# Optimization experiments

Measured on AMD Instinct MI355X. Metric: run time of the kernel, lower is better.

## Reference

```python
import jax, jax.numpy as jnp
import numpy as np

D_MODEL = 1024
N_HEADS = 16
K_TOP = 64
D_HEAD = D_MODEL // N_HEADS


def setup_inputs() -> dict:
    key = jax.random.key(0)
    ks = jax.random.split(key, 9)
    B, L = 8, 4096
    bound = 1.0 / np.sqrt(D_MODEL)  # nn.Linear default init range
    lin = lambda k: jax.random.uniform(k, (D_MODEL, D_MODEL), jnp.float32, -bound, bound)
    vec = lambda k: jax.random.uniform(k, (D_MODEL,), jnp.float32, -bound, bound)
    return {
        "query": jax.random.normal(ks[0], (B, L, D_MODEL), jnp.float32),
        "Wq": lin(ks[1]), "bq": vec(ks[2]),
        "Wk": lin(ks[3]), "bk": vec(ks[4]),
        "Wv": lin(ks[5]), "bv": vec(ks[6]),
        "Wo": lin(ks[7]), "bo": vec(ks[8]),
    }


def reference(query, Wq, bq, Wk, bk, Wv, bv, Wo, bo):
    B, L_q, D = query.shape
    L_k = L_q  # self-attention: key = value = query
    F_q = L_q // 2 + 1
    F_k = L_k // 2 + 1
    k_top = min(K_TOP, F_q)

    def proj(x, W, b):
        # (B, L, D) -> (B, H, L, d_head)
        return (x @ W + b).reshape(B, -1, N_HEADS, D_HEAD).transpose(0, 2, 1, 3)

    q = proj(query, Wq, bq)
    k = proj(query, Wk, bk)
    v = proj(query, Wv, bv)

    q_freq = jnp.fft.rfft(q, axis=2)  # (B, H, F_q, d_head) complex64
    k_freq = jnp.fft.rfft(k, axis=2)
    v_freq = jnp.fft.rfft(v, axis=2)

    # top-k frequency bins by mean spectral magnitude of the query
    q_energy = jnp.abs(q_freq).mean(axis=-1)  # (B, H, F_q)
    _, idx = jax.lax.top_k(q_energy, k_top)   # (B, H, k)
    mapped_idx = jnp.clip(
        jnp.round(idx.astype(jnp.float32) * (F_k - 1) / (F_q - 1)).astype(jnp.int32),
        0, F_k - 1)

    gather = lambda x, i: jnp.take_along_axis(x, i[..., None], axis=2)
    q_top = gather(q_freq, idx)          # (B, H, k, d_head)
    k_top_freq = gather(k_freq, mapped_idx)
    v_top = gather(v_freq, mapped_idx)

    eps = 1e-8
    attn_score = (q_top.real * k_top_freq.real).sum(-1) / (D_HEAD ** 0.5 + eps)
    attn = jax.nn.softmax(attn_score, axis=-1)[..., None]  # (B, H, k, 1)

    # fill spectrum with mean of query spectrum, then scatter attended bins
    q_mean_freq = q_freq.mean(axis=2, keepdims=True)  # (B, H, 1, d_head) complex
    out_freq = jnp.broadcast_to(q_mean_freq, (B, N_HEADS, F_q, D_HEAD))
    src = (attn * v_top.real).astype(out_freq.dtype)  # real -> complex (imag=0)
    bi = jnp.arange(B)[:, None, None]
    hi = jnp.arange(N_HEADS)[None, :, None]
    out_freq = out_freq.at[bi, hi, idx].set(src)

    out_time = jnp.fft.irfft(out_freq, n=L_q, axis=2)  # (B, H, L, d_head)
    out = out_time.transpose(0, 2, 1, 3).reshape(B, L_q, D)
    return out @ Wo + bo
```

## Files before the change

### kernel.cpp

```cpp
#include <hip/hip_runtime.h>
#include <math.h>
#include <stdint.h>


typedef _Float16 f16;
typedef _Float16 f16x8 __attribute__((ext_vector_type(8)));
typedef float f32x4 __attribute__((ext_vector_type(4)));

#define PI_F 3.14159265358979323846f
#define PADJ(j) ((j) + ((j) >> 3))

__device__ __forceinline__ void gl_lds16(const void* g, void* l) {
  __builtin_amdgcn_global_load_lds((const __attribute__((address_space(1))) void*)g,
                                   (__attribute__((address_space(3))) void*)l, 16, 0, 0);
}

__device__ __forceinline__ float2 cadd(float2 a, float2 b) { return make_float2(a.x + b.x, a.y + b.y); }
__device__ __forceinline__ float2 csub(float2 a, float2 b) { return make_float2(a.x - b.x, a.y - b.y); }
__device__ __forceinline__ float2 cmul(float2 a, float2 b) {
  return make_float2(a.x * b.x - a.y * b.y, a.x * b.y + a.y * b.x);
}
__device__ __forceinline__ float2 cmni(float2 a) { return make_float2(a.y, -a.x); }

__device__ __forceinline__ void stg4(const char* g, size_t stride, int kb, char* lds,
                                     int tid, int w, int swz) {
#pragma unroll
  for (int it = 0; it < 4; ++it) {
    int row = it * 32 + (tid >> 3);
    gl_lds16(g + (size_t)row * stride + kb + swz, lds + it * 4096 + w * 1024);
  }
}

__global__ __launch_bounds__(256) void k_tw(float2* __restrict__ twtab, float2* __restrict__ utab) {
  int j = blockIdx.x * 256 + threadIdx.x;
  if (j < 2048) {
    float ang = (float)j * (-6.28318530717958647692f / 2048.0f);
    twtab[j] = make_float2(cosf(ang), sinf(ang));
  } else if (j < 4097) {
    int f = j - 2048;
    float ang = (float)f * (-6.28318530717958647692f / 4096.0f);
    utab[f] = make_float2(cosf(ang), sinf(ang));
  }
}

__global__ __launch_bounds__(256) void k_prep(const float* __restrict__ Wq, const float* __restrict__ Wo,
                                              f16* __restrict__ WqT, f16* __restrict__ WoT) {
  __shared__ float t[32][33];
  const float* src = blockIdx.z ? Wo : Wq;
  f16* dst = blockIdx.z ? WoT : WqT;
  int c0 = blockIdx.x * 32, r0 = blockIdx.y * 32;
  int tx = threadIdx.x, ty = threadIdx.y;
#pragma unroll
  for (int yy = 0; yy < 4; ++yy)
    t[ty + yy * 8][tx] = src[(size_t)(r0 + ty + yy * 8) * 1024 + c0 + tx];
  __syncthreads();
#pragma unroll
  for (int yy = 0; yy < 4; ++yy)
    dst[(size_t)(c0 + ty + yy * 8) * 1024 + r0 + tx] = (f16)t[tx][ty + yy * 8];
}

__global__ __launch_bounds__(256) void k_prep2(const float* __restrict__ Wk, const float* __restrict__ Wv,
                                               f16* __restrict__ WkT, f16* __restrict__ WvT) {
  __shared__ float t[32][33];
  const float* src = blockIdx.z ? Wv : Wk;
  f16* dst = blockIdx.z ? WvT : WkT;
  int c0 = blockIdx.x * 32, r0 = blockIdx.y * 32;
  int tx = threadIdx.x, ty = threadIdx.y;
#pragma unroll
  for (int yy = 0; yy < 4; ++yy)
    t[ty + yy * 8][tx] = src[(size_t)(r0 + ty + yy * 8) * 1024 + c0 + tx];
  __syncthreads();
#pragma unroll
  for (int yy = 0; yy < 4; ++yy)
    dst[(size_t)(c0 + ty + yy * 8) * 1024 + r0 + tx] = (f16)t[tx][ty + yy * 8];
}

__global__ __launch_bounds__(256) void k_t1(const float* __restrict__ X, float* __restrict__ Xt) {
  __shared__ float t[32][33];
  int b = blockIdx.z;
  int l0 = blockIdx.x * 32, d0 = blockIdx.y * 32;
  int tx = threadIdx.x, ty = threadIdx.y;
#pragma unroll
  for (int yy = 0; yy < 4; ++yy)
    t[ty + yy * 8][tx] = X[((size_t)b * 4096 + l0 + ty + yy * 8) * 1024 + d0 + tx];
  __syncthreads();
#pragma unroll
  for (int yy = 0; yy < 4; ++yy)
    Xt[((size_t)b * 1024 + d0 + ty + yy * 8) * 4096 + l0 + tx] = t[tx][ty + yy * 8];
}

__device__ __forceinline__ void r8_stage(const float2* __restrict__ cur, float2* __restrict__ nxt,
                                         const float2* __restrict__ tw, int tid, int lg) {
  int Ls = 1 << lg;
  int p = tid >> lg, q = tid & (Ls - 1);
  float2 x[8];
#pragma unroll
  for (int u = 0; u < 8; ++u) x[u] = cur[PADJ(tid + 256 * u)];
  float2 s0 = cadd(x[0], x[4]), d0v = csub(x[0], x[4]);
  float2 s1 = cadd(x[2], x[6]), d1v = csub(x[2], x[6]);
  float2 e0 = cadd(s0, s1), e2 = csub(s0, s1);
  float2 md1 = cmni(d1v);
  float2 e1 = cadd(d0v, md1), e3 = csub(d0v, md1);
  float2 t0 = cadd(x[1], x[5]), u0 = csub(x[1], x[5]);
  float2 t1 = cadd(x[3], x[7]), u1 = csub(x[3], x[7]);
  float2 o0 = cadd(t0, t1), o2 = csub(t0, t1);
  float2 mu1 = cmni(u1);
  float2 o1 = cadd(u0, mu1), o3 = csub(u0, mu1);
  const float C8 = 0.70710678118654752440f;
  float2 w1 = make_float2(C8 * (o1.x + o1.y), C8 * (o1.y - o1.x));
  float2 w2 = cmni(o2);
  float2 w3 = make_float2(C8 * (o3.y - o3.x), -C8 * (o3.x + o3.y));
  float2 y[8];
  y[0] = cadd(e0, o0); y[4] = csub(e0, o0);
  y[1] = cadd(e1, w1); y[5] = csub(e1, w1);
  y[2] = cadd(e2, w2); y[6] = csub(e2, w2);
  y[3] = cadd(e3, w3); y[7] = csub(e3, w3);
  int tb = p << lg;
#pragma unroll
  for (int v = 1; v < 8; ++v) y[v] = cmul(y[v], tw[tb * v]);
  int ob = q + (p << (lg + 3));
#pragma unroll
  for (int v = 0; v < 8; ++v) nxt[PADJ(ob + (v << lg))] = y[v];
}

__global__ __launch_bounds__(256) void k_fft(const float* __restrict__ Xt,
                                             const float2* __restrict__ twtab,
                                             const float2* __restrict__ utab,
                                             f16* __restrict__ PReU, f16* __restrict__ PImU,
                                             float* __restrict__ sumXf) {
  __shared__ float2 bufA[2304];
  __shared__ float2 bufB[2304];
  __shared__ float redr[256], redi[256];
  int tid = threadIdx.x;
  int blk = blockIdx.x;

  const float4* src = (const float4*)(Xt + (size_t)blk * 4096);
#pragma unroll
  for (int r = 0; r < 4; ++r) {
    int i4 = r * 256 + tid;
    float4 v = src[i4];
    bufA[PADJ(2 * i4)] = make_float2(v.x, v.y);
    bufA[PADJ(2 * i4 + 1)] = make_float2(v.z, v.w);
  }
  __syncthreads();
  r8_stage(bufA, bufB, twtab, tid, 0);
  __syncthreads();
  r8_stage(bufB, bufA, twtab, tid, 3);
  __syncthreads();
  r8_stage(bufA, bufB, twtab, tid, 6);
  __syncthreads();
#pragma unroll
  for (int h = 0; h < 2; ++h) {
    int i = (h << 8) + tid;
    float2 a0 = bufB[PADJ(i)], a1 = bufB[PADJ(i + 512)];
    float2 a2 = bufB[PADJ(i + 1024)], a3 = bufB[PADJ(i + 1536)];
    float2 s02 = cadd(a0, a2), d02 = csub(a0, a2);
    float2 s13 = cadd(a1, a3), d13m = cmni(csub(a1, a3));
    bufA[PADJ(i)] = cadd(s02, s13);
    bufA[PADJ(i + 512)] = cadd(d02, d13m);
    bufA[PADJ(i + 1024)] = csub(s02, s13);
    bufA[PADJ(i + 1536)] = csub(d02, d13m);
  }
  __syncthreads();
  float sumr = 0.f, sumi = 0.f;
  size_t obase = (size_t)blk * 2049;
  for (int f = tid; f <= 2048; f += 256) {
    int fz = f & 2047, fm = (2048 - f) & 2047;
    float2 z = bufA[PADJ(fz)], m = bufA[PADJ(fm)];
    float Er = 0.5f * (z.x + m.x), Ei = 0.5f * (z.y - m.y);
    float Or = 0.5f * (z.y + m.y), Oi = -0.5f * (z.x - m.x);
    float2 wv = utab[f];
    float Xr = Er + wv.x * Or - wv.y * Oi;
    float Xi = Ei + wv.x * Oi + wv.y * Or;
    PReU[obase + f] = (f16)Xr;
    PImU[obase + f] = (f16)Xi;
    sumr += Xr; sumi += Xi;
  }
  __syncthreads();
  redr[tid] = sumr; redi[tid] = sumi;
  __syncthreads();
  for (int s = 128; s > 0; s >>= 1) {
    if (tid < s) { redr[tid] += redr[tid + s]; redi[tid] += redi[tid + s]; }
    __syncthreads();
  }
  if (tid == 0) { sumXf[2 * blk] = redr[0]; sumXf[2 * blk + 1] = redi[0]; }
}

__global__ __launch_bounds__(256) void k_C(const float* __restrict__ sumXf, const float* __restrict__ Wq,
                                           const float* __restrict__ bq,
                                           float* __restrict__ Cre, float* __restrict__ Cim) {
  int b = blockIdx.x >> 2;
  int hd = ((blockIdx.x & 3) << 8) + threadIdx.x;
  float accr = 0.f, acci = 0.f;
  for (int dm = 0; dm < 1024; ++dm) {
    float w = Wq[(size_t)dm * 1024 + hd];
    accr += sumXf[2 * (b * 1024 + dm)] * w;
    acci += sumXf[2 * (b * 1024 + dm) + 1] * w;
  }
  Cre[b * 1024 + hd] = (accr + 4096.0f * bq[hd]) * (1.0f / 2049.0f);
  Cim[b * 1024 + hd] = acci * (1.0f / 2049.0f);
}

__global__ __launch_bounds__(256) void k_t2(const f16* __restrict__ PReU, const f16* __restrict__ PImU,
                                            f16* __restrict__ PT) {
  __shared__ f16 t[32][33];
  int z = blockIdx.z;
  int b = z >> 1, pl = z & 1;
  const f16* src = pl ? PImU : PReU;
  int f0 = blockIdx.x * 32, d0 = blockIdx.y * 32;
  int tx = threadIdx.x, ty = threadIdx.y;
#pragma unroll
  for (int yy = 0; yy < 4; ++yy) {
    int ff = f0 + tx;
    t[ty + yy * 8][tx] = (ff < 2049) ? src[(size_t)(b * 1024 + d0 + ty + yy * 8) * 2049 + ff] : (f16)0.f;
  }
  __syncthreads();
#pragma unroll
  for (int yy = 0; yy < 4; ++yy)
    PT[((size_t)b * 4352 + 2 * (f0 + ty + yy * 8) + pl) * 1024 + d0 + tx] = t[tx][ty + yy * 8];
}

__global__ __launch_bounds__(256, 2) void k_energy(const f16* __restrict__ PT, const f16* __restrict__ WqT,
                                                   const float* __restrict__ bq, float* __restrict__ energy) {
  __shared__ __align__(16) f16 sA[2][128 * 64];
  __shared__ __align__(16) f16 sB[2][128 * 64];
  int tid = threadIdx.x;
  int lane = tid & 63, w = tid >> 6;
  int lin = blockIdx.x;
  int xq = lin & 7, rq = lin >> 3;
  int bN = rq & 7;
  int Mblk = ((rq >> 3) << 3) + xq;
  int wr = w >> 1, wc = w & 1;
  f32x4 acc[4][4];
#pragma unroll
  for (int mf = 0; mf < 4; ++mf)
#pragma unroll
    for (int nf = 0; nf < 4; ++nf) acc[mf][nf] = 0;

  const char* gA0 = (const char*)PT + (size_t)(Mblk * 128) * 2048;
  const char* gB0 = (const char*)WqT + (size_t)(bN * 128) * 2048;
  int swz = ((tid & 7) ^ ((tid >> 3) & 7)) << 4;
  int r = lane & 15, q = lane >> 4;
  int cq = q << 4;

  stg4(gA0, 2048, 0, (char*)&sA[0][0], tid, w, swz);
  stg4(gB0, 2048, 0, (char*)&sB[0][0], tid, w, swz);
  for (int ks = 0; ks < 16; ++ks) {
    int cur = ks & 1;
    if (ks < 15) {
      int kb = (ks + 1) * 128;
      stg4(gA0, 2048, kb, (char*)&sA[cur ^ 1][0], tid, w, swz);
      stg4(gB0, 2048, kb, (char*)&sB[cur ^ 1][0], tid, w, swz);
      asm volatile("s_waitcnt vmcnt(8)\ns_barrier" ::: "memory");
    } else {
      asm volatile("s_waitcnt vmcnt(0)\ns_barrier" ::: "memory");
    }
    const char* bA = (const char*)&sA[cur][0];
    const char* bB = (const char*)&sB[cur][0];
#pragma unroll
    for (int kk = 0; kk < 64; kk += 32) {
      int cb = (kk << 1) + cq;
      f16x8 aF[4], bF[4];
#pragma unroll
      for (int mf = 0; mf < 4; ++mf) {
        int row = wr * 64 + mf * 16 + r;
        aF[mf] = *(const f16x8*)(bA + row * 128 + (cb ^ ((row & 7) << 4)));
      }
#pragma unroll
      for (int nf = 0; nf < 4; ++nf) {
        int row = wc * 64 + nf * 16 + r;
        bF[nf] = *(const f16x8*)(bB + row * 128 + (cb ^ ((row & 7) << 4)));
      }
#pragma unroll
      for (int mf = 0; mf < 4; ++mf)
#pragma unroll
        for (int nf = 0; nf < 4; ++nf)
          acc[mf][nf] = __builtin_amdgcn_mfma_f32_16x16x32_f16(aF[mf], bF[nf], acc[mf][nf], 0, 0, 0);
    }
    asm volatile("s_barrier" ::: "memory");
  }
  int b = Mblk / 34;
  int tIb = Mblk - b * 34;
  int head = 2 * bN + wc;
  bool dc = (tIb == 0 && wr == 0 && q == 0);
#pragma unroll
  for (int mf = 0; mf < 4; ++mf) {
    float sE = 0.f, sO = 0.f;
#pragma unroll
    for (int nf = 0; nf < 4; ++nf) {
      float re0 = acc[mf][nf][0], im0 = acc[mf][nf][1];
      float re1 = acc[mf][nf][2], im1 = acc[mf][nf][3];
      if (dc && mf == 0) re0 += 4096.0f * bq[head * 64 + nf * 16 + r];
      sE += sqrtf(re0 * re0 + im0 * im0);
      sO += sqrtf(re1 * re1 + im1 * im1);
    }
#pragma unroll
    for (int off = 1; off < 16; off <<= 1) {
      sE += __shfl_xor(sE, off);
      sO += __shfl_xor(sO, off);
    }
    if (r == 0) {
      int fp = tIb * 64 + wr * 32 + mf * 8 + (q << 1);
      energy[((size_t)b * 16 + head) * 2176 + fp] = sE * 0.015625f;
      energy[((size_t)b * 16 + head) * 2176 + fp + 1] = sO * 0.015625f;
    }
  }
}

__global__ __launch_bounds__(256) void k_topk(const float* __restrict__ energy, int* __restrict__ idxb) {
  __shared__ float vals[2049];
  __shared__ unsigned long long wbest[4];
  int tid = threadIdx.x, bh = blockIdx.x;
  const float* e = energy + (size_t)bh * 2176;
  for (int i = tid; i < 2049; i += 256) vals[i] = e[i];
  __syncthreads();
  for (int it = 0; it < 64; ++it) {
    unsigned long long best = 0ull;
    for (int f = tid; f < 2049; f += 256) {
      unsigned b32 = __float_as_uint(vals[f]);
      b32 = (b32 & 0x80000000u) ? ~b32 : (b32 | 0x80000000u);
      unsigned long long k = ((unsigned long long)b32 << 12) | (unsigned)(4095 - f);
      best = (k > best) ? k : best;
    }
#pragma unroll
    for (int off = 32; off > 0; off >>= 1) {
      unsigned long long o = __shfl_xor(best, off);
      best = (o > best) ? o : best;
    }
    if ((tid & 63) == 0) wbest[tid >> 6] = best;
    __syncthreads();
    if (tid == 0) {
      unsigned long long b0 = wbest[0] > wbest[1] ? wbest[0] : wbest[1];
      unsigned long long b1 = wbest[2] > wbest[3] ? wbest[2] : wbest[3];
      unsigned long long bb = b0 > b1 ? b0 : b1;
      int f = 4095 - (int)(bb & 4095ull);
      idxb[bh * 64 + it] = f;
      vals[f] = -1.0f;
    }
    __syncthreads();
  }
}

__global__ __launch_bounds__(256) void k_qkv(const f16* __restrict__ PT, const int* __restrict__ idxb,
                                             const f16* __restrict__ WqT, const f16* __restrict__ WkT,
                                             const f16* __restrict__ WvT, float* __restrict__ part) {
  __shared__ __align__(16) f16 sA[64 * 64];
  __shared__ __align__(16) f16 sB[192 * 64];
  __shared__ int fjs[64];
  int tid = threadIdx.x, lane = tid & 63, w = tid >> 6;
  int bh = blockIdx.x, ks = blockIdx.y;
  int b = bh >> 4, h = bh & 15;
  if (tid < 64) fjs[tid] = idxb[bh * 64 + tid];
  __syncthreads();
  f32x4 acc[4][3];
#pragma unroll
  for (int mf = 0; mf < 4; ++mf)
#pragma unroll
    for (int nf = 0; nf < 3; ++nf) acc[mf][nf] = 0;

  int l8 = lane & 7;
  int lr = lane >> 3;
  int swz = (l8 ^ lr) << 4;

  for (int kt = 0; kt < 4; ++kt) {
    int kbyte = ks * 512 + kt * 128;
#pragma unroll
    for (int t = 0; t < 2; ++t) {
      int ia = w * 2 + t;
      int row = ia * 8 + lr;
      const char* src = (const char*)PT + (size_t)(b * 4352 + 2 * fjs[row]) * 2048 + kbyte + swz;
      gl_lds16(src, (char*)sA + ia * 1024);
    }
#pragma unroll
    for (int t = 0; t < 6; ++t) {
      int ib = w * 6 + t;
      int row = ib * 8 + lr;
      const f16* Wt = (row < 64) ? WqT : (row < 128) ? WkT : WvT;
      const char* src = (const char*)Wt + (size_t)(h * 64 + (row & 63)) * 2048 + kbyte + swz;
      gl_lds16(src, (char*)sB + ib * 1024);
    }
    __syncthreads();
#pragma unroll
    for (int kk = 0; kk < 64; kk += 32) {
      int cb = (kk << 1) + ((lane >> 4) << 4);
      int r = lane & 15;
      f16x8 aF[4], bF[3];
#pragma unroll
      for (int mf = 0; mf < 4; ++mf) {
        int row = mf * 16 + r;
        aF[mf] = *(const f16x8*)((const char*)sA + row * 128 + (cb ^ ((row & 7) << 4)));
      }
#pragma unroll
      for (int nf = 0; nf < 3; ++nf) {
        int row = w * 48 + nf * 16 + r;
        bF[nf] = *(const f16x8*)((const char*)sB + row * 128 + (cb ^ ((row & 7) << 4)));
      }
#pragma unroll
      for (int mf = 0; mf < 4; ++mf)
#pragma unroll
        for (int nf = 0; nf < 3; ++nf)
          acc[mf][nf] = __builtin_amdgcn_mfma_f32_16x16x32_f16(aF[mf], bF[nf], acc[mf][nf], 0, 0, 0);
    }
    __syncthreads();
  }
  float* pb = part + (size_t)(ks * 128 + bh) * 12288;
#pragma unroll
  for (int mf = 0; mf < 4; ++mf)
#pragma unroll
    for (int nf = 0; nf < 3; ++nf)
#pragma unroll
      for (int rr = 0; rr < 4; ++rr) {
        int m = mf * 16 + ((lane >> 4) << 2) + rr;
        int n = w * 48 + nf * 16 + (lane & 15);
        pb[m * 192 + n] = acc[mf][nf][rr];
      }
}

__global__ __launch_bounds__(256) void k_attn2(const float* __restrict__ part, const int* __restrict__ idxb,
                                               const float* __restrict__ bq, const float* __restrict__ bk,
                                               const float* __restrict__ bv, const float* __restrict__ Cre,
                                               f16* __restrict__ ampT) {
  __shared__ float sQKV[64][196];
  __shared__ float scores[64], attns[64];
  __shared__ int fjs[64];
  __shared__ int dcrow;
  int tid = threadIdx.x, bh = blockIdx.x;
  int b = bh >> 4, h = bh & 15;
  if (tid == 0) dcrow = -1;
  __syncthreads();
  if (tid < 64) {
    int f = idxb[bh * 64 + tid];
    fjs[tid] = f;
    if (f == 0) dcrow = tid;
  }
  __syncthreads();
  const float4* p0 = (const float4*)(part + (size_t)bh * 12288);
  const size_t s4 = (size_t)128 * 12288 / 4;
#pragma unroll
  for (int it = 0; it < 12; ++it) {
    int e = it * 256 + tid;
    float4 v0 = p0[e], v1 = p0[e + s4], v2 = p0[e + 2 * s4], v3 = p0[e + 3 * s4];
    float4 v;
    v.x = v0.x + v1.x + v2.x + v3.x;
    v.y = v0.y + v1.y + v2.y + v3.y;
    v.z = v0.z + v1.z + v2.z + v3.z;
    v.w = v0.w + v1.w + v2.w + v3.w;
    int m = e / 48, n0 = (e % 48) * 4;
    *(float4*)&sQKV[m][n0] = v;
  }
  __syncthreads();
  if (dcrow >= 0 && tid < 192) {
    const float* bias = (tid < 64) ? bq : (tid < 128) ? bk : bv;
    sQKV[dcrow][tid] += 4096.0f * bias[h * 64 + (tid & 63)];
  }
  __syncthreads();
  {
    int j = tid >> 2, p = tid & 3;
    float s = 0.f;
#pragma unroll
    for (int c = 0; c < 16; ++c) {
      int cc = p * 16 + c;
      s = fmaf(sQKV[j][cc], sQKV[j][64 + cc], s);
    }
    s += __shfl_xor(s, 1);
    s += __shfl_xor(s, 2);
    if (p == 0) scores[j] = s * 0.125f;
  }
  __syncthreads();
  if (tid < 64) {
    float s = scores[tid];
    float m = s;
#pragma unroll
    for (int off = 32; off > 0; off >>= 1) m = fmaxf(m, __shfl_xor(m, off));
    float ev = expf(s - m);
    float sm = ev;
#pragma unroll
    for (int off = 32; off > 0; off >>= 1) sm += __shfl_xor(sm, off);
    attns[tid] = ev / sm;
  }
  __syncthreads();
  {
    int j = tid >> 2, d0 = (tid & 3) * 16;
    float at = attns[j];
    int fj = fjs[j];
    float wj = (fj == 0 || fj == 2048) ? 0.5f : 1.0f;
#pragma unroll
    for (int q4 = 0; q4 < 4; ++q4) {
      float4 c4 = *(const float4*)&Cre[b * 1024 + h * 64 + d0 + q4 * 4];
      float4 vv = *(const float4*)&sQKV[j][128 + d0 + q4 * 4];
      float av0 = wj * (at * vv.x - c4.x);
      float av1 = wj * (at * vv.y - c4.y);
      float av2 = wj * (at * vv.z - c4.z);
      float av3 = wj * (at * vv.w - c4.w);
      f16* o = ampT + (size_t)bh * 4096 + (d0 + q4 * 4) * 64 + j;
      o[0] = (f16)av0; o[64] = (f16)av1; o[128] = (f16)av2; o[192] = (f16)av3;
    }
  }
}

__global__ __launch_bounds__(256) void k_ot(const f16* __restrict__ ampT, const int* __restrict__ idxb,
                                            const float* __restrict__ Cre, const float* __restrict__ Cim,
                                            f16* __restrict__ OT) {
  __shared__ __align__(16) f16 sAmp[64][72];
  __shared__ float gbuf[256];
  __shared__ int fjs[64];
  int tid = threadIdx.x, lane = tid & 63, w = tid >> 6;
  int bh = blockIdx.x >> 4, tch = blockIdx.x & 15;
  int b = bh >> 4, h = bh & 15;
  if (tid < 64) fjs[tid] = idxb[bh * 64 + tid];
  {
    int row = tid >> 2, seg = tid & 3;
    const f16* src = ampT + (size_t)bh * 4096 + row * 64 + seg * 16;
    f16x8 v0 = *(const f16x8*)src;
    f16x8 v1 = *(const f16x8*)(src + 8);
    *(f16x8*)&sAmp[row][seg * 16] = v0;
    *(f16x8*)&sAmp[row][seg * 16 + 8] = v1;
  }
  __syncthreads();
  int r = lane & 15, q = lane >> 4;
  int tbase = tch * 256 + w * 64;
  const float cang = 0.00153398078788564123f;
  f16x8 aF[4][2];
  float ss[4];
#pragma unroll
  for (int mf = 0; mf < 4; ++mf) {
    int t = tbase + mf * 16 + r;
    float s = 0.f;
#pragma unroll
    for (int kk2 = 0; kk2 < 2; ++kk2) {
      f16x8 a;
#pragma unroll
      for (int jj = 0; jj < 8; ++jj) {
        int j = kk2 * 32 + q * 8 + jj;
        int ridx = (fjs[j] * t) & 4095;
        float sn, cs;
        __sincosf((float)ridx * cang, &sn, &cs);
        s += sn;
        a[jj] = (f16)cs;
      }
      aF[mf][kk2] = a;
    }
    ss[mf] = s;
  }
#pragma unroll
  for (int mf = 0; mf < 4; ++mf) {
    ss[mf] += __shfl_xor(ss[mf], 16);
    ss[mf] += __shfl_xor(ss[mf], 32);
  }
  if (q == 0) {
#pragma unroll
    for (int mf = 0; mf < 4; ++mf) {
      int t = tbase + mf * 16 + r;
      float g = ss[mf];
      if (t & 1) {
        int tp = (t <= 2048) ? t : 4096 - t;
        float sg = (t <= 2048) ? 1.f : -1.f;
        float aa = (float)tp * (PI_F / 4096.0f);
        g -= sg * (cosf(aa) / sinf(aa));
      }
      gbuf[w * 64 + mf * 16 + r] = g;
    }
  }
  f16x8 bF[4][2];
#pragma unroll
  for (int nf = 0; nf < 4; ++nf)
#pragma unroll
    for (int kk2 = 0; kk2 < 2; ++kk2)
      bF[nf][kk2] = *(const f16x8*)&sAmp[nf * 16 + r][kk2 * 32 + q * 8];
  f32x4 acc[4][4];
#pragma unroll
  for (int mf = 0; mf < 4; ++mf)
#pragma unroll
    for (int nf = 0; nf < 4; ++nf) acc[mf][nf] = 0;
#pragma unroll
  for (int kk2 = 0; kk2 < 2; ++kk2)
#pragma unroll
    for (int mf = 0; mf < 4; ++mf)
#pragma unroll
      for (int nf = 0; nf < 4; ++nf)
        acc[mf][nf] = __builtin_amdgcn_mfma_f32_16x16x32_f16(aF[mf][kk2], bF[nf][kk2], acc[mf][nf], 0, 0, 0);
  __syncthreads();
  const float s2L = 2.0f / 4096.0f;
#pragma unroll
  for (int nf = 0; nf < 4; ++nf) {
    int d = nf * 16 + r;
    float cim = Cim[b * 1024 + h * 64 + d];
    float cre = Cre[b * 1024 + h * 64 + d];
#pragma unroll
    for (int mf = 0; mf < 4; ++mf) {
#pragma unroll
      for (int rr = 0; rr < 4; ++rr) {
        int ro = mf * 16 + q * 4 + rr;
        int t = tbase + ro;
        float g = gbuf[w * 64 + ro];
        float val = s2L * (acc[mf][nf][rr] + cim * g) + ((t == 0) ? cre : 0.f);
        OT[((size_t)bh * 4096 + t) * 64 + d] = (f16)val;
      }
    }
  }
}

__global__ __launch_bounds__(256, 2) void k_final(const f16* __restrict__ OT, const f16* __restrict__ WoT,
                                                  const float* __restrict__ bo, float* __restrict__ out) {
  __shared__ __align__(16) f16 sA[2][128 * 64];
  __shared__ __align__(16) f16 sB[2][128 * 64];
  int tid = threadIdx.x, lane = tid & 63, wv = tid >> 6;
  int lin = blockIdx.x;
  int xq = lin & 7, rq = lin >> 3;
  int bN = rq & 7;
  int Mblk = ((rq >> 3) << 3) + xq;
  int wr = wv >> 1, wc = wv & 1;
  f32x4 acc[4][4];
#pragma unroll
  for (int mf = 0; mf < 4; ++mf)
#pragma unroll
    for (int nf = 0; nf < 4; ++nf) acc[mf][nf] = 0;
  int b = Mblk >> 5, t0 = (Mblk & 31) * 128;
  const char* gB0 = (const char*)WoT + (size_t)(bN * 128) * 2048;
  int swz = ((tid & 7) ^ ((tid >> 3) & 7)) << 4;
  int r = lane & 15, q = lane >> 4;
  int cq = q << 4;
#define GA_TILE(ks) ((const char*)OT + (size_t)((b * 16 + (ks)) * 4096 + t0) * 128)

  stg4(GA_TILE(0), 128, 0, (char*)&sA[0][0], tid, wv, swz);
  stg4(gB0, 2048, 0, (char*)&sB[0][0], tid, wv, swz);
  for (int ks = 0; ks < 16; ++ks) {
    int cur = ks & 1;
    if (ks < 15) {
      stg4(GA_TILE(ks + 1), 128, 0, (char*)&sA[cur ^ 1][0], tid, wv, swz);
      stg4(gB0, 2048, (ks + 1) * 128, (char*)&sB[cur ^ 1][0], tid, wv, swz);
      asm volatile("s_waitcnt vmcnt(8)\ns_barrier" ::: "memory");
    } else {
      asm volatile("s_waitcnt vmcnt(0)\ns_barrier" ::: "memory");
    }
    const char* bA = (const char*)&sA[cur][0];
    const char* bB = (const char*)&sB[cur][0];
#pragma unroll
    for (int kk = 0; kk < 64; kk += 32) {
      int cb = (kk << 1) + cq;
      f16x8 aF[4], bF[4];
#pragma unroll
      for (int mf = 0; mf < 4; ++mf) {
        int row = wr * 64 + mf * 16 + r;
        aF[mf] = *(const f16x8*)(bA + row * 128 + (cb ^ ((row & 7) << 4)));
      }
#pragma unroll
      for (int nf = 0; nf < 4; ++nf) {
        int row = wc * 64 + nf * 16 + r;
        bF[nf] = *(const f16x8*)(bB + row * 128 + (cb ^ ((row & 7) << 4)));
      }
#pragma unroll
      for (int mf = 0; mf < 4; ++mf)
#pragma unroll
        for (int nf = 0; nf < 4; ++nf)
          acc[mf][nf] = __builtin_amdgcn_mfma_f32_16x16x32_f16(aF[mf], bF[nf], acc[mf][nf], 0, 0, 0);
    }
    asm volatile("s_barrier" ::: "memory");
  }
#undef GA_TILE
#pragma unroll
  for (int nf = 0; nf < 4; ++nf) {
    int gcol = bN * 128 + wc * 64 + nf * 16 + r;
    float bcol = bo[gcol];
#pragma unroll
    for (int mf = 0; mf < 4; ++mf) {
#pragma unroll
      for (int rr = 0; rr < 4; ++rr) {
        int grow = Mblk * 128 + wr * 64 + mf * 16 + (q << 2) + rr;
        out[(size_t)grow * 1024 + gcol] = acc[mf][nf][rr] + bcol;
      }
    }
  }
}

extern "C" void kernel_launch(void* const* d_in, const int* in_sizes, int n_in,
                              void* d_out, int out_size, void* d_ws, size_t ws_size,
                              hipStream_t stream) {
  const float* X = (const float*)d_in[0];
  const float* Wq = (const float*)d_in[1];
  const float* bq = (const float*)d_in[2];
  const float* Wk = (const float*)d_in[3];
  const float* bk = (const float*)d_in[4];
  const float* Wv = (const float*)d_in[5];
  const float* bv = (const float*)d_in[6];
  const float* Wo = (const float*)d_in[7];
  const float* bo = (const float*)d_in[8];
  float* out = (float*)d_out;

  if (ws_size < 208928768ULL) return;
  char* w = (char*)d_ws;
  float* Xt = (float*)(w);
  f16* PT = (f16*)(w);
  f16* WkT = (f16*)(w + 71303168);
  f16* WvT = (f16*)(w + 73400320);
  float* part = (float*)(w + 75497472);
  char* R2 = w + 134217728;
  f16* PReU = (f16*)(R2);
  f16* PImU = (f16*)(R2 + 33570816);
  f16* OT = (f16*)(R2);
  char* R3 = R2 + 67141632;
  float* sumXf = (float*)(R3);
  float* Cre = (float*)(R3 + 65536);
  float* Cim = (float*)(R3 + 98304);
  float* energy = (float*)(R3 + 131072);
  int* idxb = (int*)(R3 + 1245184);
  f16* ampT = (f16*)(R3 + 1277952);
  f16* WqT = (f16*)(R3 + 3375104);
  f16* WoT = (f16*)(R3 + 5472256);
  float2* twtab = (float2*)d_out;
  float2* utab = twtab + 2048;

  dim3 b32(32, 8);
  hipLaunchKernelGGL(k_tw, dim3(17), dim3(256), 0, stream, twtab, utab);
  hipLaunchKernelGGL(k_prep, dim3(32, 32, 2), b32, 0, stream, Wq, Wo, WqT, WoT);
  hipLaunchKernelGGL(k_t1, dim3(128, 32, 8), b32, 0, stream, X, Xt);
  hipLaunchKernelGGL(k_fft, dim3(8192), dim3(256), 0, stream, Xt, twtab, utab, PReU, PImU, sumXf);
  hipLaunchKernelGGL(k_prep2, dim3(32, 32, 2), b32, 0, stream, Wk, Wv, WkT, WvT);
  hipLaunchKernelGGL(k_C, dim3(32), dim3(256), 0, stream, sumXf, Wq, bq, Cre, Cim);
  hipLaunchKernelGGL(k_t2, dim3(68, 32, 16), b32, 0, stream, PReU, PImU, PT);
  hipLaunchKernelGGL(k_energy, dim3(2176), dim3(256), 0, stream, PT, WqT, bq, energy);
  hipLaunchKernelGGL(k_topk, dim3(128), dim3(256), 0, stream, energy, idxb);
  hipLaunchKernelGGL(k_qkv, dim3(128, 4), dim3(256), 0, stream, PT, idxb, WqT, WkT, WvT, part);
  hipLaunchKernelGGL(k_attn2, dim3(128), dim3(256), 0, stream, part, idxb, bq, bk, bv, Cre, ampT);
  hipLaunchKernelGGL(k_ot, dim3(2048), dim3(256), 0, stream, ampT, idxb, Cre, Cim, OT);
  hipLaunchKernelGGL(k_final, dim3(2048), dim3(256), 0, stream, OT, WoT, bo, out);
}
```

Measured before the change: 526.8 us.

## Widen GEMM tiles to 128x256 with K-step 32 in energy and final kernels

Both the energy GEMM and the output-projection GEMM move from 128x128 tiles with K-step 64 to 128x256 tiles with K-step 32. Each wave now holds a 64x128 accumulator and issues 32 MFMAs per stage, and LDS swizzling is changed to a 4-slot XOR pattern. Block swizzling is reworked for the halved grid sizes. This raises arithmetic intensity per LDS load and halves A-tile refetches. The cost is higher register pressure (128 accumulator floats) and twice as many barrier-synchronised stages.

```diff
diff --git a/kernel.cpp b/kernel.cpp
--- a/kernel.cpp
+++ b/kernel.cpp
@@ -22,12 +22,20 @@
 }
 __device__ __forceinline__ float2 cmni(float2 a) { return make_float2(a.y, -a.x); }
 
-__device__ __forceinline__ void stg4(const char* g, size_t stride, int kb, char* lds,
-                                     int tid, int w, int swz) {
-#pragma unroll
-  for (int it = 0; it < 4; ++it) {
-    int row = it * 32 + (tid >> 3);
-    gl_lds16(g + (size_t)row * stride + kb + swz, lds + it * 4096 + w * 1024);
+__device__ __forceinline__ void stgA(const char* g, size_t stride, int kb, char* lds, int tid, int w) {
+#pragma unroll
+  for (int i = 0; i < 2; ++i) {
+    int row = i * 64 + (tid >> 2);
+    int slot = tid & 3;
+    gl_lds16(g + (size_t)row * stride + kb + ((slot ^ (row & 3)) << 4), lds + i * 4096 + w * 1024);
+  }
+}
+__device__ __forceinline__ void stgB(const char* g, size_t stride, int kb, char* lds, int tid, int w) {
+#pragma unroll
+  for (int i = 0; i < 4; ++i) {
+    int row = i * 64 + (tid >> 2);
+    int slot = tid & 3;
+    gl_lds16(g + (size_t)row * stride + kb + ((slot ^ (row & 3)) << 4), lds + i * 4096 + w * 1024);
   }
 }
 
@@ -222,87 +230,85 @@
 
 __global__ __launch_bounds__(256, 2) void k_energy(const f16* __restrict__ PT, const f16* __restrict__ WqT,
                                                    const float* __restrict__ bq, float* __restrict__ energy) {
-  __shared__ __align__(16) f16 sA[2][128 * 64];
-  __shared__ __align__(16) f16 sB[2][128 * 64];
+  __shared__ __align__(16) f16 sA[2][128 * 32];
+  __shared__ __align__(16) f16 sB[2][256 * 32];
   int tid = threadIdx.x;
   int lane = tid & 63, w = tid >> 6;
   int lin = blockIdx.x;
-  int xq = lin & 7, rq = lin >> 3;
-  int bN = rq & 7;
-  int Mblk = ((rq >> 3) << 3) + xq;
+  int sw = (lin & 7) * 136 + (lin >> 3);
+  int bN = sw & 3, Mblk = sw >> 2;
   int wr = w >> 1, wc = w & 1;
-  f32x4 acc[4][4];
+  f32x4 acc[4][8];
 #pragma unroll
   for (int mf = 0; mf < 4; ++mf)
 #pragma unroll
-    for (int nf = 0; nf < 4; ++nf) acc[mf][nf] = 0;
+    for (int nf = 0; nf < 8; ++nf) acc[mf][nf] = 0;
 
   const char* gA0 = (const char*)PT + (size_t)(Mblk * 128) * 2048;
-  const char* gB0 = (const char*)WqT + (size_t)(bN * 128) * 2048;
-  int swz = ((tid & 7) ^ ((tid >> 3) & 7)) << 4;
+  const char* gB0 = (const char*)WqT + (size_t)(bN * 256) * 2048;
   int r = lane & 15, q = lane >> 4;
-  int cq = q << 4;
-
-  stg4(gA0, 2048, 0, (char*)&sA[0][0], tid, w, swz);
-  stg4(gB0, 2048, 0, (char*)&sB[0][0], tid, w, swz);
-  for (int ks = 0; ks < 16; ++ks) {
+
+  stgA(gA0, 2048, 0, (char*)&sA[0][0], tid, w);
+  stgB(gB0, 2048, 0, (char*)&sB[0][0], tid, w);
+  for (int ks = 0; ks < 32; ++ks) {
     int cur = ks & 1;
-    if (ks < 15) {
-      int kb = (ks + 1) * 128;
-      stg4(gA0, 2048, kb, (char*)&sA[cur ^ 1][0], tid, w, swz);
-      stg4(gB0, 2048, kb, (char*)&sB[cur ^ 1][0], tid, w, swz);
-      asm volatile("s_waitcnt vmcnt(8)\ns_barrier" ::: "memory");
+    if (ks < 31) {
+      int kb = (ks + 1) * 64;
+      stgA(gA0, 2048, kb, (char*)&sA[cur ^ 1][0], tid, w);
+      stgB(gB0, 2048, kb, (char*)&sB[cur ^ 1][0], tid, w);
+      asm volatile("s_waitcnt vmcnt(6)\ns_barrier" ::: "memory");
     } else {
       asm volatile("s_waitcnt vmcnt(0)\ns_barrier" ::: "memory");
     }
     const char* bA = (const char*)&sA[cur][0];
     const char* bB = (const char*)&sB[cur][0];
-#pragma unroll
-    for (int kk = 0; kk < 64; kk += 32) {
-      int cb = (kk << 1) + cq;
-      f16x8 aF[4], bF[4];
-#pragma unroll
-      for (int mf = 0; mf < 4; ++mf) {
-        int row = wr * 64 + mf * 16 + r;
-        aF[mf] = *(const f16x8*)(bA + row * 128 + (cb ^ ((row & 7) << 4)));
-      }
-#pragma unroll
-      for (int nf = 0; nf < 4; ++nf) {
-        int row = wc * 64 + nf * 16 + r;
-        bF[nf] = *(const f16x8*)(bB + row * 128 + (cb ^ ((row & 7) << 4)));
-      }
-#pragma unroll
-      for (int mf = 0; mf < 4; ++mf)
-#pragma unroll
-        for (int nf = 0; nf < 4; ++nf)
-          acc[mf][nf] = __builtin_amdgcn_mfma_f32_16x16x32_f16(aF[mf], bF[nf], acc[mf][nf], 0, 0, 0);
-    }
+    f16x8 aF[4], bF[8];
+#pragma unroll
+    for (int mf = 0; mf < 4; ++mf) {
+      int row = wr * 64 + mf * 16 + r;
+      aF[mf] = *(const f16x8*)(bA + row * 64 + ((q ^ (row & 3)) << 4));
+    }
+#pragma unroll
+    for (int nf = 0; nf < 8; ++nf) {
+      int row = wc * 128 + nf * 16 + r;
+      bF[nf] = *(const f16x8*)(bB + row * 64 + ((q ^ (row & 3)) << 4));
+    }
+#pragma unroll
+    for (int mf = 0; mf < 4; ++mf)
+#pragma unroll
+      for (int nf = 0; nf < 8; ++nf)
+        acc[mf][nf] = __builtin_amdgcn_mfma_f32_16x16x32_f16(aF[mf], bF[nf], acc[mf][nf], 0, 0, 0);
     asm volatile("s_barrier" ::: "memory");
   }
   int b = Mblk / 34;
   int tIb = Mblk - b * 34;
-  int head = 2 * bN + wc;
-  bool dc = (tIb == 0 && wr == 0 && q == 0);
+  int h0 = bN * 4 + wc * 2;
+  bool dc0 = (tIb == 0 && wr == 0 && q == 0);
 #pragma unroll
   for (int mf = 0; mf < 4; ++mf) {
-    float sE = 0.f, sO = 0.f;
-#pragma unroll
-    for (int nf = 0; nf < 4; ++nf) {
+    float sE0 = 0.f, sO0 = 0.f, sE1 = 0.f, sO1 = 0.f;
+#pragma unroll
+    for (int nf = 0; nf < 8; ++nf) {
       float re0 = acc[mf][nf][0], im0 = acc[mf][nf][1];
       float re1 = acc[mf][nf][2], im1 = acc[mf][nf][3];
-      if (dc && mf == 0) re0 += 4096.0f * bq[head * 64 + nf * 16 + r];
-      sE += sqrtf(re0 * re0 + im0 * im0);
-      sO += sqrtf(re1 * re1 + im1 * im1);
+      if (dc0 && mf == 0) re0 += 4096.0f * bq[(h0 + (nf >> 2)) * 64 + (nf & 3) * 16 + r];
+      float m0 = sqrtf(re0 * re0 + im0 * im0);
+      float m1 = sqrtf(re1 * re1 + im1 * im1);
+      if (nf < 4) { sE0 += m0; sO0 += m1; } else { sE1 += m0; sO1 += m1; }
     }
 #pragma unroll
     for (int off = 1; off < 16; off <<= 1) {
-      sE += __shfl_xor(sE, off);
-      sO += __shfl_xor(sO, off);
+      sE0 += __shfl_xor(sE0, off);
+      sO0 += __shfl_xor(sO0, off);
+      sE1 += __shfl_xor(sE1, off);
+      sO1 += __shfl_xor(sO1, off);
     }
     if (r == 0) {
       int fp = tIb * 64 + wr * 32 + mf * 8 + (q << 1);
-      energy[((size_t)b * 16 + head) * 2176 + fp] = sE * 0.015625f;
-      energy[((size_t)b * 16 + head) * 2176 + fp + 1] = sO * 0.015625f;
+      energy[((size_t)b * 16 + h0) * 2176 + fp] = sE0 * 0.015625f;
+      energy[((size_t)b * 16 + h0) * 2176 + fp + 1] = sO0 * 0.015625f;
+      energy[((size_t)b * 16 + h0 + 1) * 2176 + fp] = sE1 * 0.015625f;
+      energy[((size_t)b * 16 + h0 + 1) * 2176 + fp + 1] = sO1 * 0.015625f;
     }
   }
 }
@@ -602,65 +608,58 @@
 
 __global__ __launch_bounds__(256, 2) void k_final(const f16* __restrict__ OT, const f16* __restrict__ WoT,
                                                   const float* __restrict__ bo, float* __restrict__ out) {
-  __shared__ __align__(16) f16 sA[2][128 * 64];
-  __shared__ __align__(16) f16 sB[2][128 * 64];
-  int tid = threadIdx.x, lane = tid & 63, wv = tid >> 6;
+  __shared__ __align__(16) f16 sA[2][128 * 32];
+  __shared__ __align__(16) f16 sB[2][256 * 32];
+  int tid = threadIdx.x, lane = tid & 63, w = tid >> 6;
   int lin = blockIdx.x;
-  int xq = lin & 7, rq = lin >> 3;
-  int bN = rq & 7;
-  int Mblk = ((rq >> 3) << 3) + xq;
-  int wr = wv >> 1, wc = wv & 1;
-  f32x4 acc[4][4];
+  int sw = (lin & 7) * 128 + (lin >> 3);
+  int bN = sw & 3, Mblk = sw >> 2;
+  int wr = w >> 1, wc = w & 1;
+  f32x4 acc[4][8];
 #pragma unroll
   for (int mf = 0; mf < 4; ++mf)
 #pragma unroll
-    for (int nf = 0; nf < 4; ++nf) acc[mf][nf] = 0;
+    for (int nf = 0; nf < 8; ++nf) acc[mf][nf] = 0;
   int b = Mblk >> 5, t0 = (Mblk & 31) * 128;
-  const char* gB0 = (const char*)WoT + (size_t)(bN * 128) * 2048;
-  int swz = ((tid & 7) ^ ((tid >> 3) & 7)) << 4;
+  const char* gB0 = (const char*)WoT + (size_t)(bN * 256) * 2048;
   int r = lane & 15, q = lane >> 4;
-  int cq = q << 4;
-#define GA_TILE(ks) ((const char*)OT + (size_t)((b * 16 + (ks)) * 4096 + t0) * 128)
-
-  stg4(GA_TILE(0), 128, 0, (char*)&sA[0][0], tid, wv, swz);
-  stg4(gB0, 2048, 0, (char*)&sB[0][0], tid, wv, swz);
-  for (int ks = 0; ks < 16; ++ks) {
+#define GA_HEAD(ks) ((const char*)OT + ((size_t)(b * 16 + ((ks) >> 1)) * 4096 + t0) * 128)
+
+  stgA(GA_HEAD(0), 128, 0, (char*)&sA[0][0], tid, w);
+  stgB(gB0, 2048, 0, (char*)&sB[0][0], tid, w);
+  for (int ks = 0; ks < 32; ++ks) {
     int cur = ks & 1;
-    if (ks < 15) {
-      stg4(GA_TILE(ks + 1), 128, 0, (char*)&sA[cur ^ 1][0], tid, wv, swz);
-      stg4(gB0, 2048, (ks + 1) * 128, (char*)&sB[cur ^ 1][0], tid, wv, swz);
-      asm volatile("s_waitcnt vmcnt(8)\ns_barrier" ::: "memory");
+    if (ks < 31) {
+      stgA(GA_HEAD(ks + 1), 128, ((ks + 1) & 1) * 64, (char*)&sA[cur ^ 1][0], tid, w);
+      stgB(gB0, 2048, (ks + 1) * 64, (char*)&sB[cur ^ 1][0], tid, w);
+      asm volatile("s_waitcnt vmcnt(6)\ns_barrier" ::: "memory");
     } else {
       asm volatile("s_waitcnt vmcnt(0)\ns_barrier" ::: "memory");
     }
     const char* bA = (const char*)&sA[cur][0];
     const char* bB = (const char*)&sB[cur][0];
-#pragma unroll
-    for (int kk = 0; kk < 64; kk += 32) {
-      int cb = (kk << 1) + cq;
-      f16x8 aF[4], bF[4];
-#pragma unroll
-      for (int mf = 0; mf < 4; ++mf) {
-        int row = wr * 64 + mf * 16 + r;
-        aF[mf] = *(const f16x8*)(bA + row * 128 + (cb ^ ((row & 7) << 4)));
-      }
-#pragma unroll
-      for (int nf = 0; nf < 4; ++nf) {
-        int row = wc * 64 + nf * 16 + r;
-        bF[nf] = *(const f16x8*)(bB + row * 128 + (cb ^ ((row & 7) << 4)));
-      }
-#pragma unroll
-      for (int mf = 0; mf < 4; ++mf)
-#pragma unroll
-        for (int nf = 0; nf < 4; ++nf)
-          acc[mf][nf] = __builtin_amdgcn_mfma_f32_16x16x32_f16(aF[mf], bF[nf], acc[mf][nf], 0, 0, 0);
-    }
+    f16x8 aF[4], bF[8];
+#pragma unroll
+    for (int mf = 0; mf < 4; ++mf) {
+      int row = wr * 64 + mf * 16 + r;
+      aF[mf] = *(const f16x8*)(bA + row * 64 + ((q ^ (row & 3)) << 4));
+    }
+#pragma unroll
+    for (int nf = 0; nf < 8; ++nf) {
+      int row = wc * 128 + nf * 16 + r;
+      bF[nf] = *(const f16x8*)(bB + row * 64 + ((q ^ (row & 3)) << 4));
+    }
+#pragma unroll
+    for (int mf = 0; mf < 4; ++mf)
+#pragma unroll
+      for (int nf = 0; nf < 8; ++nf)
+        acc[mf][nf] = __builtin_amdgcn_mfma_f32_16x16x32_f16(aF[mf], bF[nf], acc[mf][nf], 0, 0, 0);
     asm volatile("s_barrier" ::: "memory");
   }
-#undef GA_TILE
-#pragma unroll
-  for (int nf = 0; nf < 4; ++nf) {
-    int gcol = bN * 128 + wc * 64 + nf * 16 + r;
+#undef GA_HEAD
+#pragma unroll
+  for (int nf = 0; nf < 8; ++nf) {
+    int gcol = bN * 256 + wc * 128 + nf * 16 + r;
     float bcol = bo[gcol];
 #pragma unroll
     for (int mf = 0; mf < 4; ++mf) {
@@ -718,10 +717,10 @@
   hipLaunchKernelGGL(k_prep2, dim3(32, 32, 2), b32, 0, stream, Wk, Wv, WkT, WvT);
   hipLaunchKernelGGL(k_C, dim3(32), dim3(256), 0, stream, sumXf, Wq, bq, Cre, Cim);
   hipLaunchKernelGGL(k_t2, dim3(68, 32, 16), b32, 0, stream, PReU, PImU, PT);
-  hipLaunchKernelGGL(k_energy, dim3(2176), dim3(256), 0, stream, PT, WqT, bq, energy);
+  hipLaunchKernelGGL(k_energy, dim3(1088), dim3(256), 0, stream, PT, WqT, bq, energy);
   hipLaunchKernelGGL(k_topk, dim3(128), dim3(256), 0, stream, energy, idxb);
   hipLaunchKernelGGL(k_qkv, dim3(128, 4), dim3(256), 0, stream, PT, idxb, WqT, WkT, WvT, part);
   hipLaunchKernelGGL(k_attn2, dim3(128), dim3(256), 0, stream, part, idxb, bq, bk, bv, Cre, ampT);
   hipLaunchKernelGGL(k_ot, dim3(2048), dim3(256), 0, stream, ampT, idxb, Cre, Cim, OT);
-  hipLaunchKernelGGL(k_final, dim3(2048), dim3(256), 0, stream, OT, WoT, bo, out);
-}
+  hipLaunchKernelGGL(k_final, dim3(1024), dim3(256), 0, stream, OT, WoT, bo, out);
+}
```

Measured after the change: 539.1 us. 1.02x slower.
